# Optimization experiments

Hardware: AMD Instinct MI355X
Metric: run time of the kernel (lower is better)

Reference implementation:

```python
import jax, jax.numpy as jnp
import numpy as np

D_MODEL, H, D_FF = 512, 8, 2048
DK = D_MODEL // H
EPS = 1e-5  # torch LayerNorm default


def layer_norm(x, g, b):
    m = jnp.mean(x, axis=-1, keepdims=True)
    v = jnp.mean((x - m) ** 2, axis=-1, keepdims=True)
    return (x - m) * jax.lax.rsqrt(v + EPS) * g + b


def setup_inputs() -> dict:
    key = jax.random.key(0)
    ks = jax.random.split(key, 10)
    B, S = 8, 2048
    s = lambda fan_in: 1.0 / np.sqrt(fan_in)
    return {
        "x": jax.random.normal(ks[0], (B, S, D_MODEL), jnp.float32),
        # per-head projections stacked: [h, d_model, dk] (bias-free Project)
        "wq": jax.random.uniform(ks[1], (H, D_MODEL, DK), jnp.float32, -s(D_MODEL), s(D_MODEL)),
        "wk": jax.random.uniform(ks[2], (H, D_MODEL, DK), jnp.float32, -s(D_MODEL), s(D_MODEL)),
        "wv": jax.random.uniform(ks[3], (H, D_MODEL, DK), jnp.float32, -s(D_MODEL), s(D_MODEL)),
        "wo": jax.random.uniform(ks[4], (D_MODEL, D_MODEL), jnp.float32, -s(D_MODEL), s(D_MODEL)),
        "w1": jax.random.uniform(ks[5], (D_MODEL, D_FF), jnp.float32, -s(D_MODEL), s(D_MODEL)),
        "b1": jax.random.uniform(ks[6], (D_FF,), jnp.float32, -s(D_MODEL), s(D_MODEL)),
        "w2": jax.random.uniform(ks[7], (D_FF, D_MODEL), jnp.float32, -s(D_FF), s(D_FF)),
        "b2": jax.random.uniform(ks[8], (D_MODEL,), jnp.float32, -s(D_FF), s(D_FF)),
        "ln1_g": jnp.ones((D_MODEL,), jnp.float32),
        "ln1_b": jnp.zeros((D_MODEL,), jnp.float32),
        "ln2_g": jnp.ones((D_MODEL,), jnp.float32),
        "ln2_b": jnp.zeros((D_MODEL,), jnp.float32),
    }


def reference(x, wq, wk, wv, wo, w1, b1, w2, b2, ln1_g, ln1_b, ln2_g, ln2_b):
    B, S, D = x.shape
    # --- multi-head self-attention (8 per-head Linears fused into one einsum) ---
    q = jnp.einsum("bsd,hdk->bhsk", x, wq)
    k = jnp.einsum("bsd,hdk->bhsk", x, wk)
    v = jnp.einsum("bsd,hdk->bhsk", x, wv)
    score = jnp.einsum("bhsk,bhtk->bhst", q, k) * (1.0 / np.sqrt(DK))
    attn = jax.nn.softmax(score, axis=-1)
    heads = jnp.einsum("bhst,bhtk->bhsk", attn, v)
    concat = heads.transpose(0, 2, 1, 3).reshape(B, S, D)  # cat over heads
    mha = concat @ wo
    # dropout in eval mode -> identity
    x = layer_norm(mha + x, ln1_g, ln1_b)
    # --- feed-forward ---
    ffn = jax.nn.relu(x @ w1 + b1) @ w2 + b2
    return layer_norm(ffn + x, ln2_g, ln2_b)
```

## Files before the change

### kernel.cpp

```cpp
#include <hip/hip_runtime.h>
#include <hip/hip_bf16.h>
#include <math.h>


#define D_MODEL 512
#define NHEAD   8
#define DKH     64
#define SEQ     2048
#define BATCH   8
#define DFF     2048
#define MROWS   (BATCH * SEQ)
#define QKVLD   1536

typedef __bf16 bf16x8 __attribute__((ext_vector_type(8)));
typedef float  f32x4  __attribute__((ext_vector_type(4)));

__device__ __forceinline__ unsigned short f2bf(float f) {
    union { float f; unsigned u; } v; v.f = f;
    return (unsigned short)((v.u + 0x7FFFu + ((v.u >> 16) & 1u)) >> 16);
}

__device__ __forceinline__ unsigned cvtpk(float a, float b) {
    unsigned r;
    asm("v_cvt_pk_bf16_f32 %0, %1, %2" : "=v"(r) : "v"(a), "v"(b));
    return r;
}

__device__ __forceinline__ float fexp2(float x) {
    float r; asm("v_exp_f32 %0, %1" : "=v"(r) : "v"(x)); return r;
}

__device__ __forceinline__ f32x4 mfma16(bf16x8 a, bf16x8 b, f32x4 c) {
    return __builtin_amdgcn_mfma_f32_16x16x32_bf16(a, b, c, 0, 0, 0);
}

__device__ __forceinline__ void gld_lds16(const unsigned short* g, unsigned short* l) {
    __builtin_amdgcn_global_load_lds(
        (const __attribute__((address_space(1))) unsigned int*)g,
        (__attribute__((address_space(3))) unsigned int*)l, 16, 0, 0);
}

template<bool BIAS, bool RELU, bool RES, bool OUTF32>
__global__ __launch_bounds__(256)
void mfma_gemm(const unsigned short* __restrict__ Av,
               const unsigned short* __restrict__ Bt,
               const float* __restrict__ bias, const float* __restrict__ res,
               void* __restrict__ Cv, int Kdim, int lda, int ldc)
{
    __shared__ unsigned short As[2][128][32];
    __shared__ unsigned short Bs[2][128][32];

    const int tid  = threadIdx.x;
    const int lane = tid & 63;
    const int w    = tid >> 6;
    const int mq   = (w >> 1) << 6;
    const int nq   = (w & 1) << 6;
    const int lrow = lane & 15;
    const int g    = lane >> 4;
    const int lk   = g << 3;

    const int row0 = blockIdx.y << 7;
    const int col0 = blockIdx.x << 7;

    const int c0   = w << 5;
    const int srow = lane >> 2;
    const int scol = (lane & 3) << 3;
    const size_t aoff = (size_t)(row0 + c0 + srow) * lda  + scol;
    const size_t boff = (size_t)(col0 + c0 + srow) * Kdim + scol;

    auto stage = [&](int buf, int kt) {
        gld_lds16(Av + aoff + kt,                        &As[buf][c0     ][0]);
        gld_lds16(Av + aoff + (size_t)16 * lda  + kt,    &As[buf][c0 + 16][0]);
        gld_lds16(Bt + boff + kt,                        &Bs[buf][c0     ][0]);
        gld_lds16(Bt + boff + (size_t)16 * Kdim + kt,    &Bs[buf][c0 + 16][0]);
    };

    const f32x4 zero = {0.f, 0.f, 0.f, 0.f};
    f32x4 acc[4][4];
    #pragma unroll
    for (int i = 0; i < 4; ++i)
        #pragma unroll
        for (int j = 0; j < 4; ++j) acc[i][j] = zero;

    stage(0, 0);
    __syncthreads();

    int cur = 0;
    for (int kt = 0; kt < Kdim; kt += 32) {
        if (kt + 32 < Kdim) stage(cur ^ 1, kt + 32);

        bf16x8 af[4], bfv[4];
        #pragma unroll
        for (int mf = 0; mf < 4; ++mf)
            af[mf] = *(const bf16x8*)&As[cur][mq + mf * 16 + lrow][lk];
        #pragma unroll
        for (int nf = 0; nf < 4; ++nf)
            bfv[nf] = *(const bf16x8*)&Bs[cur][nq + nf * 16 + lrow][lk];
        #pragma unroll
        for (int mf = 0; mf < 4; ++mf)
            #pragma unroll
            for (int nf = 0; nf < 4; ++nf)
                acc[mf][nf] = mfma16(af[mf], bfv[nf], acc[mf][nf]);

        __syncthreads();
        cur ^= 1;
    }

    const int orow = row0 + mq + g * 4;
    const int ocol = col0 + nq + lrow;
    #pragma unroll
    for (int mf = 0; mf < 4; ++mf) {
        #pragma unroll
        for (int nf = 0; nf < 4; ++nf) {
            const int cc = ocol + nf * 16;
            float bv = 0.f;
            if constexpr (BIAS) bv = bias[cc];
            float v[4];
            #pragma unroll
            for (int r = 0; r < 4; ++r) {
                const int rr = orow + mf * 16 + r;
                v[r] = acc[mf][nf][r];
                if constexpr (BIAS) v[r] += bv;
                if constexpr (RELU) v[r] = fmaxf(v[r], 0.f);
                if constexpr (RES)  v[r] += res[(size_t)rr * ldc + cc];
                if constexpr (OUTF32) ((float*)Cv)[(size_t)rr * ldc + cc] = v[r];
            }
            if constexpr (!OUTF32) {
                const unsigned u01 = cvtpk(v[0], v[1]);
                const unsigned u23 = cvtpk(v[2], v[3]);
                unsigned short* cp = (unsigned short*)Cv + (size_t)(orow + mf * 16) * ldc + cc;
                cp[0]                 = (unsigned short)u01;
                cp[(size_t)ldc]       = (unsigned short)(u01 >> 16);
                cp[(size_t)ldc * 2]   = (unsigned short)u23;
                cp[(size_t)ldc * 3]   = (unsigned short)(u23 >> 16);
            }
        }
    }
}

__device__ __forceinline__ void softmax_store(
    f32x4* sacc, float* mrun, float* lpart, f32x4* oacc,
    unsigned short (*Ps)[76], int rowbase, int g, int lrow)
{
    float pmax[4];
    bool need = false;
    #pragma unroll
    for (int r = 0; r < 4; ++r) {
        pmax[r] = fmaxf(fmaxf(sacc[0][r], sacc[1][r]),
                        fmaxf(sacc[2][r], sacc[3][r]));
        need |= (pmax[r] > mrun[r] + 8.f);
    }
    if (__any(need)) {
        #pragma unroll
        for (int r = 0; r < 4; ++r) {
            float mt = pmax[r];
            mt = fmaxf(mt, __shfl_xor(mt, 1, 16));
            mt = fmaxf(mt, __shfl_xor(mt, 2, 16));
            mt = fmaxf(mt, __shfl_xor(mt, 4, 16));
            mt = fmaxf(mt, __shfl_xor(mt, 8, 16));
            const float mnew = fmaxf(mrun[r], mt);
            const float alpha = fexp2(mrun[r] - mnew);
            mrun[r] = mnew;
            lpart[r] *= alpha;
            #pragma unroll
            for (int nf = 0; nf < 4; ++nf) oacc[nf][r] *= alpha;
        }
    }
    #pragma unroll
    for (int r = 0; r < 4; ++r) {
        const float p0 = fexp2(sacc[0][r] - mrun[r]);
        const float p1 = fexp2(sacc[1][r] - mrun[r]);
        const float p2 = fexp2(sacc[2][r] - mrun[r]);
        const float p3 = fexp2(sacc[3][r] - mrun[r]);
        lpart[r] += (p0 + p1) + (p2 + p3);
        uint2 u;
        u.x = cvtpk(p0, p1);
        u.y = cvtpk(p2, p3);
        *(uint2*)&Ps[rowbase + g * 4 + r][4 * lrow] = u;
    }
}

__global__ __launch_bounds__(512, 4)
void mfma_attn(unsigned short* __restrict__ qkv)
{
    __shared__ unsigned short Ks[64][72];
    __shared__ unsigned short Vt[64][72];
    __shared__ unsigned short Ps[256][76];

    const int tid  = threadIdx.x;
    const int lane = tid & 63;
    const int w    = tid >> 6;
    const int lrow = lane & 15;
    const int g    = lane >> 4;
    const int lk   = g << 3;

    const int bid  = blockIdx.x;
    const int idx  = bid >> 3;
    const int bh   = (bid & 7) * 8 + (idx & 7);
    const int b  = bh >> 3, h = bh & 7;
    const int s0 = (idx >> 3) << 8;

    unsigned short* qptr = qkv + ((size_t)(b * SEQ + s0)) * QKVLD + h * DKH;
    const unsigned short* kbase = qkv + ((size_t)(b * SEQ)) * QKVLD + 512 + h * DKH;
    const unsigned short* vbase = qkv + ((size_t)(b * SEQ)) * QKVLD + 1024 + h * DKH;

    bf16x8 qf[2][2];
    #pragma unroll
    for (int sub = 0; sub < 2; ++sub) {
        const unsigned short* qp = qptr + (size_t)(w * 32 + sub * 16 + lrow) * QKVLD;
        qf[sub][0] = *(const bf16x8*)(qp + lk);
        qf[sub][1] = *(const bf16x8*)(qp + 32 + lk);
    }

    const int kr = tid >> 3, kc = (tid & 7) << 3;
    const int vr = tid & 63, vc = (tid >> 6) << 3;
    const int cvr = ((vr & 15) << 2) | (vr >> 4);

    uint4 kreg, vreg;
    auto loadKV = [&](int t0) {
        kreg = *(const uint4*)(kbase + (size_t)(t0 + kr) * QKVLD + kc);
        vreg = *(const uint4*)(vbase + (size_t)(t0 + vr) * QKVLD + vc);
    };
    loadKV(0);

    const f32x4 zero = {0.f, 0.f, 0.f, 0.f};
    f32x4 oacc0[4], oacc1[4];
    float m0[4], l0[4], m1[4], l1[4];
    #pragma unroll
    for (int i = 0; i < 4; ++i) {
        oacc0[i] = zero; oacc1[i] = zero;
        m0[i] = -INFINITY; m1[i] = -INFINITY; l0[i] = 0.f; l1[i] = 0.f;
    }

    for (int t0 = 0; t0 < SEQ; t0 += 64) {
        __syncthreads();
        *(uint4*)&Ks[kr][kc] = kreg;
        {
            const unsigned short* vu = (const unsigned short*)&vreg;
            #pragma unroll
            for (int j = 0; j < 8; ++j) Vt[vc + j][cvr] = vu[j];
        }
        __syncthreads();

        if (t0 + 64 < SEQ) loadKV(t0 + 64);

        f32x4 s0a[4], s1a[4];
        #pragma unroll
        for (int nf = 0; nf < 4; ++nf) { s0a[nf] = zero; s1a[nf] = zero; }
        __builtin_amdgcn_s_setprio(1);
        #pragma unroll
        for (int kk = 0; kk < 2; ++kk) {
            #pragma unroll
            for (int nf = 0; nf < 4; ++nf) {
                const bf16x8 kf = *(const bf16x8*)&Ks[nf * 16 + lrow][kk * 32 + lk];
                s0a[nf] = mfma16(qf[0][kk], kf, s0a[nf]);
                s1a[nf] = mfma16(qf[1][kk], kf, s1a[nf]);
            }
        }
        __builtin_amdgcn_s_setprio(0);

        softmax_store(s0a, m0, l0, oacc0, Ps, w * 32,      g, lrow);
        softmax_store(s1a, m1, l1, oacc1, Ps, w * 32 + 16, g, lrow);

        __builtin_amdgcn_s_setprio(1);
        #pragma unroll
        for (int kk = 0; kk < 2; ++kk) {
            const bf16x8 pf0 = *(const bf16x8*)&Ps[w * 32 + lrow][kk * 32 + lk];
            const bf16x8 pf1 = *(const bf16x8*)&Ps[w * 32 + 16 + lrow][kk * 32 + lk];
            #pragma unroll
            for (int nf = 0; nf < 4; ++nf) {
                const bf16x8 vf = *(const bf16x8*)&Vt[nf * 16 + lrow][kk * 32 + lk];
                oacc0[nf] = mfma16(pf0, vf, oacc0[nf]);
                oacc1[nf] = mfma16(pf1, vf, oacc1[nf]);
            }
        }
        __builtin_amdgcn_s_setprio(0);
    }

    #pragma unroll
    for (int r = 0; r < 4; ++r) {
        float l = l0[r];
        l += __shfl_xor(l, 1, 16);
        l += __shfl_xor(l, 2, 16);
        l += __shfl_xor(l, 4, 16);
        l += __shfl_xor(l, 8, 16);
        const float inv = 1.f / l;
        #pragma unroll
        for (int nf = 0; nf < 4; ++nf)
            qptr[(size_t)(w * 32 + g * 4 + r) * QKVLD + nf * 16 + lrow] =
                f2bf(oacc0[nf][r] * inv);
    }
    #pragma unroll
    for (int r = 0; r < 4; ++r) {
        float l = l1[r];
        l += __shfl_xor(l, 1, 16);
        l += __shfl_xor(l, 2, 16);
        l += __shfl_xor(l, 4, 16);
        l += __shfl_xor(l, 8, 16);
        const float inv = 1.f / l;
        #pragma unroll
        for (int nf = 0; nf < 4; ++nf)
            qptr[(size_t)(w * 32 + 16 + g * 4 + r) * QKVLD + nf * 16 + lrow] =
                f2bf(oacc1[nf][r] * inv);
    }
}

template<bool WB>
__global__ __launch_bounds__(256)
void ln_kernel(const float* __restrict__ in, const float* __restrict__ gg,
               const float* __restrict__ bb, float* __restrict__ outf,
               unsigned short* __restrict__ outb)
{
    const int row = blockIdx.x * 4 + (threadIdx.x >> 6);
    const int lane = threadIdx.x & 63;
    const float* p = in + (size_t)row * D_MODEL;

    const float4 a = *(const float4*)(p + lane * 4);
    const float4 c = *(const float4*)(p + 256 + lane * 4);
    float sum = a.x + a.y + a.z + a.w + c.x + c.y + c.z + c.w;
    float sq  = a.x*a.x + a.y*a.y + a.z*a.z + a.w*a.w
              + c.x*c.x + c.y*c.y + c.z*c.z + c.w*c.w;
    #pragma unroll
    for (int msk = 1; msk < 64; msk <<= 1) {
        sum += __shfl_xor(sum, msk, 64);
        sq  += __shfl_xor(sq,  msk, 64);
    }
    const float mean = sum * (1.f / 512.f);
    const float var  = sq * (1.f / 512.f) - mean * mean;
    const float rs   = rsqrtf(var + 1e-5f);

    const float4 g0 = *(const float4*)(gg + lane * 4);
    const float4 g1 = *(const float4*)(gg + 256 + lane * 4);
    const float4 b0 = *(const float4*)(bb + lane * 4);
    const float4 b1 = *(const float4*)(bb + 256 + lane * 4);

    float4 o0, o1;
    o0.x = (a.x - mean) * rs * g0.x + b0.x;
    o0.y = (a.y - mean) * rs * g0.y + b0.y;
    o0.z = (a.z - mean) * rs * g0.z + b0.z;
    o0.w = (a.w - mean) * rs * g0.w + b0.w;
    o1.x = (c.x - mean) * rs * g1.x + b1.x;
    o1.y = (c.y - mean) * rs * g1.y + b1.y;
    o1.z = (c.z - mean) * rs * g1.z + b1.z;
    o1.w = (c.w - mean) * rs * g1.w + b1.w;
    *(float4*)(outf + (size_t)row * D_MODEL + lane * 4) = o0;
    *(float4*)(outf + (size_t)row * D_MODEL + 256 + lane * 4) = o1;
    if constexpr (WB) {
        uint2 pa, pb;
        pa.x = cvtpk(o0.x, o0.y);
        pa.y = cvtpk(o0.z, o0.w);
        pb.x = cvtpk(o1.x, o1.y);
        pb.y = cvtpk(o1.z, o1.w);
        *(uint2*)(outb + (size_t)row * D_MODEL + lane * 4) = pa;
        *(uint2*)(outb + (size_t)row * D_MODEL + 256 + lane * 4) = pb;
    }
}

__global__ __launch_bounds__(256)
void cast_bf16(const float* __restrict__ in, unsigned short* __restrict__ out)
{
    const size_t i = ((size_t)blockIdx.x * 256 + threadIdx.x) * 8;
    const float4 a = *(const float4*)(in + i);
    const float4 b = *(const float4*)(in + i + 4);
    uint4 o;
    o.x = cvtpk(a.x, a.y);
    o.y = cvtpk(a.z, a.w);
    o.z = cvtpk(b.x, b.y);
    o.w = cvtpk(b.z, b.w);
    *(uint4*)(out + i) = o;
}

__global__ __launch_bounds__(256)
void pack_qkv(const float* __restrict__ wq, const float* __restrict__ wk,
              const float* __restrict__ wv, unsigned short* __restrict__ Wqkv)
{
    const int idx = blockIdx.x * 256 + threadIdx.x;
    const int n = idx >> 9, d = idx & 511;
    const int h = n >> 6, c = n & 63;
    const size_t src = ((size_t)h * 512 + d) * 64 + c;
    Wqkv[idx]                 = f2bf(wq[src] * 0.18033688f);
    Wqkv[idx + 512 * 512]     = f2bf(wk[src]);
    Wqkv[idx + 2 * 512 * 512] = f2bf(wv[src]);
}

__global__ __launch_bounds__(256)
void pack_t(const float* __restrict__ in, unsigned short* __restrict__ out,
            int K, int N)
{
    const int idx = blockIdx.x * 256 + threadIdx.x;
    const int n = idx / K, k = idx % K;
    out[idx] = f2bf(in[(size_t)k * N + n]);
}

extern "C" void kernel_launch(void* const* d_in, const int* in_sizes, int n_in,
                              void* d_out, int out_size, void* d_ws, size_t ws_size,
                              hipStream_t stream)
{
    (void)in_sizes; (void)n_in; (void)out_size;

    const float* x    = (const float*)d_in[0];
    const float* wq   = (const float*)d_in[1];
    const float* wk   = (const float*)d_in[2];
    const float* wv   = (const float*)d_in[3];
    const float* wo   = (const float*)d_in[4];
    const float* w1   = (const float*)d_in[5];
    const float* b1   = (const float*)d_in[6];
    const float* w2   = (const float*)d_in[7];
    const float* b2   = (const float*)d_in[8];
    const float* ln1g = (const float*)d_in[9];
    const float* ln1b = (const float*)d_in[10];
    const float* ln2g = (const float*)d_in[11];
    const float* ln2b = (const float*)d_in[12];
    float* out = (float*)d_out;

    const size_t QKV_BYTES = (size_t)MROWS * QKVLD * 2;
    const size_t Y_BYTES   = (size_t)MROWS * D_MODEL * 4;
    unsigned char* base = (unsigned char*)d_ws;
    unsigned short* qkv  = (unsigned short*)(base);
    float*          y    = (float*)(base + QKV_BYTES);
    unsigned short* Wqkv = (unsigned short*)(base + QKV_BYTES + Y_BYTES);
    unsigned short* wo_t = Wqkv + 3 * 512 * 512;
    unsigned short* w1_t = wo_t + 512 * 512;
    unsigned short* w2_t = w1_t + 2048 * 512;
    unsigned short* hid  = w2_t + 2048 * 512;

    const size_t hid_off = (size_t)((unsigned char*)hid - base);
    const size_t avail = (ws_size > hid_off) ? (ws_size - hid_off) : 0;
    int chunk = (int)(avail / ((size_t)DFF * 2));
    chunk &= ~127;
    if (chunk > MROWS) chunk = MROWS;
    if (chunk < 128)   chunk = 128;

    float* y2 = (float*)qkv;
    unsigned short* xb  = (unsigned short*)d_out;
    unsigned short* x1b = (unsigned short*)d_out;

    pack_qkv<<<1024, 256, 0, stream>>>(wq, wk, wv, Wqkv);
    pack_t<<<(512 * 512) / 256, 256, 0, stream>>>(wo, wo_t, 512, 512);
    pack_t<<<(2048 * 512) / 256, 256, 0, stream>>>(w1, w1_t, 512, 2048);
    pack_t<<<(2048 * 512) / 256, 256, 0, stream>>>(w2, w2_t, 2048, 512);
    cast_bf16<<<(MROWS * D_MODEL) / (256 * 8), 256, 0, stream>>>(x, xb);

    const dim3 blk(256);

    mfma_gemm<false, false, false, false>
        <<<dim3(12, MROWS / 128), blk, 0, stream>>>(xb, Wqkv, nullptr, nullptr,
                                                    qkv, 512, 512, QKVLD);

    mfma_attn<<<dim3(512), dim3(512), 0, stream>>>(qkv);

    mfma_gemm<false, false, true, true>
        <<<dim3(4, MROWS / 128), blk, 0, stream>>>(qkv, wo_t, nullptr, x, y,
                                                   512, QKVLD, 512);

    ln_kernel<true><<<MROWS / 4, blk, 0, stream>>>(y, ln1g, ln1b, y, x1b);

    for (int r0 = 0; r0 < MROWS; r0 += chunk) {
        const int rows = (r0 + chunk <= MROWS) ? chunk : (MROWS - r0);
        mfma_gemm<true, true, false, false>
            <<<dim3(DFF / 128, rows / 128), blk, 0, stream>>>(
                x1b + (size_t)r0 * D_MODEL, w1_t, b1, nullptr, hid,
                512, 512, DFF);
        mfma_gemm<true, false, true, true>
            <<<dim3(4, rows / 128), blk, 0, stream>>>(
                hid, w2_t, b2, y + (size_t)r0 * D_MODEL,
                y2 + (size_t)r0 * D_MODEL, DFF, DFF, 512);
    }

    ln_kernel<false><<<MROWS / 4, blk, 0, stream>>>(y2, ln2g, ln2b, out, nullptr);
}
```

Baseline: 311.7 us.

## Widen GEMM tiles, load attention K directly, use bf16 residual, tiled weight transpose

Adds a templated N-tile width so the QKV and FFN1 GEMMs use 128x256 tiles, raising data reuse per block. The attention kernel reads K fragments directly from global memory into registers, dropping the K shared-memory staging and its barrier traffic. LN1 stops writing its fp32 output and the FFN2 epilogue adds the residual from the bf16 copy, cutting memory traffic at some precision cost. The weight transpose kernels now use a shared-memory tile so both reads and writes are coalesced.

```diff
diff --git a/kernel.cpp b/kernel.cpp
--- a/kernel.cpp
+++ b/kernel.cpp
@@ -20,6 +20,11 @@
     return (unsigned short)((v.u + 0x7FFFu + ((v.u >> 16) & 1u)) >> 16);
 }
 
+__device__ __forceinline__ float bf2f(unsigned short u) {
+    union { unsigned u; float f; } v; v.u = (unsigned)u << 16;
+    return v.f;
+}
+
 __device__ __forceinline__ unsigned cvtpk(float a, float b) {
     unsigned r;
     asm("v_cvt_pk_bf16_f32 %0, %1, %2" : "=v"(r) : "v"(a), "v"(b));
@@ -40,47 +45,51 @@
         (__attribute__((address_space(3))) unsigned int*)l, 16, 0, 0);
 }
 
-template<bool BIAS, bool RELU, bool RES, bool OUTF32>
+template<int NF, bool BIAS, bool RELU, int RESMODE, bool OUTF32>
 __global__ __launch_bounds__(256)
 void mfma_gemm(const unsigned short* __restrict__ Av,
                const unsigned short* __restrict__ Bt,
-               const float* __restrict__ bias, const float* __restrict__ res,
+               const float* __restrict__ bias, const void* __restrict__ resv,
                void* __restrict__ Cv, int Kdim, int lda, int ldc)
 {
+    constexpr int BN = NF * 32;
     __shared__ unsigned short As[2][128][32];
-    __shared__ unsigned short Bs[2][128][32];
+    __shared__ unsigned short Bs[2][BN][32];
 
     const int tid  = threadIdx.x;
     const int lane = tid & 63;
     const int w    = tid >> 6;
     const int mq   = (w >> 1) << 6;
-    const int nq   = (w & 1) << 6;
+    const int nq   = (w & 1) * (NF * 16);
     const int lrow = lane & 15;
     const int g    = lane >> 4;
     const int lk   = g << 3;
 
     const int row0 = blockIdx.y << 7;
-    const int col0 = blockIdx.x << 7;
-
-    const int c0   = w << 5;
+    const int col0 = blockIdx.x * BN;
+
+    const int c0a  = w << 5;
+    const int c0b  = w * (BN / 4);
     const int srow = lane >> 2;
     const int scol = (lane & 3) << 3;
-    const size_t aoff = (size_t)(row0 + c0 + srow) * lda  + scol;
-    const size_t boff = (size_t)(col0 + c0 + srow) * Kdim + scol;
+    const size_t aoff = (size_t)(row0 + c0a + srow) * lda  + scol;
+    const size_t boff = (size_t)(col0 + c0b + srow) * Kdim + scol;
 
     auto stage = [&](int buf, int kt) {
-        gld_lds16(Av + aoff + kt,                        &As[buf][c0     ][0]);
-        gld_lds16(Av + aoff + (size_t)16 * lda  + kt,    &As[buf][c0 + 16][0]);
-        gld_lds16(Bt + boff + kt,                        &Bs[buf][c0     ][0]);
-        gld_lds16(Bt + boff + (size_t)16 * Kdim + kt,    &Bs[buf][c0 + 16][0]);
+        gld_lds16(Av + aoff + kt,                     &As[buf][c0a     ][0]);
+        gld_lds16(Av + aoff + (size_t)16 * lda + kt,  &As[buf][c0a + 16][0]);
+        #pragma unroll
+        for (int j = 0; j < BN / 64; ++j)
+            gld_lds16(Bt + boff + (size_t)(16 * j) * Kdim + kt,
+                      &Bs[buf][c0b + 16 * j][0]);
     };
 
     const f32x4 zero = {0.f, 0.f, 0.f, 0.f};
-    f32x4 acc[4][4];
+    f32x4 acc[4][NF];
     #pragma unroll
     for (int i = 0; i < 4; ++i)
         #pragma unroll
-        for (int j = 0; j < 4; ++j) acc[i][j] = zero;
+        for (int j = 0; j < NF; ++j) acc[i][j] = zero;
 
     stage(0, 0);
     __syncthreads();
@@ -89,18 +98,17 @@
     for (int kt = 0; kt < Kdim; kt += 32) {
         if (kt + 32 < Kdim) stage(cur ^ 1, kt + 32);
 
-        bf16x8 af[4], bfv[4];
+        bf16x8 af[4];
         #pragma unroll
         for (int mf = 0; mf < 4; ++mf)
             af[mf] = *(const bf16x8*)&As[cur][mq + mf * 16 + lrow][lk];
         #pragma unroll
-        for (int nf = 0; nf < 4; ++nf)
-            bfv[nf] = *(const bf16x8*)&Bs[cur][nq + nf * 16 + lrow][lk];
-        #pragma unroll
-        for (int mf = 0; mf < 4; ++mf)
-            #pragma unroll
-            for (int nf = 0; nf < 4; ++nf)
-                acc[mf][nf] = mfma16(af[mf], bfv[nf], acc[mf][nf]);
+        for (int nf = 0; nf < NF; ++nf) {
+            const bf16x8 bf = *(const bf16x8*)&Bs[cur][nq + nf * 16 + lrow][lk];
+            #pragma unroll
+            for (int mf = 0; mf < 4; ++mf)
+                acc[mf][nf] = mfma16(af[mf], bf, acc[mf][nf]);
+        }
 
         __syncthreads();
         cur ^= 1;
@@ -111,7 +119,7 @@
     #pragma unroll
     for (int mf = 0; mf < 4; ++mf) {
         #pragma unroll
-        for (int nf = 0; nf < 4; ++nf) {
+        for (int nf = 0; nf < NF; ++nf) {
             const int cc = ocol + nf * 16;
             float bv = 0.f;
             if constexpr (BIAS) bv = bias[cc];
@@ -122,7 +130,10 @@
                 v[r] = acc[mf][nf][r];
                 if constexpr (BIAS) v[r] += bv;
                 if constexpr (RELU) v[r] = fmaxf(v[r], 0.f);
-                if constexpr (RES)  v[r] += res[(size_t)rr * ldc + cc];
+                if constexpr (RESMODE == 1)
+                    v[r] += ((const float*)resv)[(size_t)rr * ldc + cc];
+                if constexpr (RESMODE == 2)
+                    v[r] += bf2f(((const unsigned short*)resv)[(size_t)rr * ldc + cc]);
                 if constexpr (OUTF32) ((float*)Cv)[(size_t)rr * ldc + cc] = v[r];
             }
             if constexpr (!OUTF32) {
@@ -183,7 +194,6 @@
 __global__ __launch_bounds__(512, 4)
 void mfma_attn(unsigned short* __restrict__ qkv)
 {
-    __shared__ unsigned short Ks[64][72];
     __shared__ unsigned short Vt[64][72];
     __shared__ unsigned short Ps[256][76];
 
@@ -212,16 +222,14 @@
         qf[sub][1] = *(const bf16x8*)(qp + 32 + lk);
     }
 
-    const int kr = tid >> 3, kc = (tid & 7) << 3;
     const int vr = tid & 63, vc = (tid >> 6) << 3;
     const int cvr = ((vr & 15) << 2) | (vr >> 4);
 
-    uint4 kreg, vreg;
-    auto loadKV = [&](int t0) {
-        kreg = *(const uint4*)(kbase + (size_t)(t0 + kr) * QKVLD + kc);
+    uint4 vreg;
+    auto loadV = [&](int t0) {
         vreg = *(const uint4*)(vbase + (size_t)(t0 + vr) * QKVLD + vc);
     };
-    loadKV(0);
+    loadV(0);
 
     const f32x4 zero = {0.f, 0.f, 0.f, 0.f};
     f32x4 oacc0[4], oacc1[4];
@@ -233,8 +241,15 @@
     }
 
     for (int t0 = 0; t0 < SEQ; t0 += 64) {
+        bf16x8 kf[2][4];
+        #pragma unroll
+        for (int kk = 0; kk < 2; ++kk)
+            #pragma unroll
+            for (int nf = 0; nf < 4; ++nf)
+                kf[kk][nf] = *(const bf16x8*)(
+                    kbase + (size_t)(t0 + nf * 16 + lrow) * QKVLD + kk * 32 + lk);
+
         __syncthreads();
-        *(uint4*)&Ks[kr][kc] = kreg;
         {
             const unsigned short* vu = (const unsigned short*)&vreg;
             #pragma unroll
@@ -242,7 +257,7 @@
         }
         __syncthreads();
 
-        if (t0 + 64 < SEQ) loadKV(t0 + 64);
+        if (t0 + 64 < SEQ) loadV(t0 + 64);
 
         f32x4 s0a[4], s1a[4];
         #pragma unroll
@@ -252,9 +267,8 @@
         for (int kk = 0; kk < 2; ++kk) {
             #pragma unroll
             for (int nf = 0; nf < 4; ++nf) {
-                const bf16x8 kf = *(const bf16x8*)&Ks[nf * 16 + lrow][kk * 32 + lk];
-                s0a[nf] = mfma16(qf[0][kk], kf, s0a[nf]);
-                s1a[nf] = mfma16(qf[1][kk], kf, s1a[nf]);
+                s0a[nf] = mfma16(qf[0][kk], kf[kk][nf], s0a[nf]);
+                s1a[nf] = mfma16(qf[1][kk], kf[kk][nf], s1a[nf]);
             }
         }
         __builtin_amdgcn_s_setprio(0);
@@ -305,7 +319,7 @@
     }
 }
 
-template<bool WB>
+template<bool WF32, bool WB16>
 __global__ __launch_bounds__(256)
 void ln_kernel(const float* __restrict__ in, const float* __restrict__ gg,
                const float* __restrict__ bb, float* __restrict__ outf,
@@ -343,9 +357,11 @@
     o1.y = (c.y - mean) * rs * g1.y + b1.y;
     o1.z = (c.z - mean) * rs * g1.z + b1.z;
     o1.w = (c.w - mean) * rs * g1.w + b1.w;
-    *(float4*)(outf + (size_t)row * D_MODEL + lane * 4) = o0;
-    *(float4*)(outf + (size_t)row * D_MODEL + 256 + lane * 4) = o1;
-    if constexpr (WB) {
+    if constexpr (WF32) {
+        *(float4*)(outf + (size_t)row * D_MODEL + lane * 4) = o0;
+        *(float4*)(outf + (size_t)row * D_MODEL + 256 + lane * 4) = o1;
+    }
+    if constexpr (WB16) {
         uint2 pa, pb;
         pa.x = cvtpk(o0.x, o0.y);
         pa.y = cvtpk(o0.z, o0.w);
@@ -387,9 +403,16 @@
 void pack_t(const float* __restrict__ in, unsigned short* __restrict__ out,
             int K, int N)
 {
-    const int idx = blockIdx.x * 256 + threadIdx.x;
-    const int n = idx / K, k = idx % K;
-    out[idx] = f2bf(in[(size_t)k * N + n]);
+    __shared__ float t[32][33];
+    const int kb = blockIdx.x << 5, nb = blockIdx.y << 5;
+    const int c = threadIdx.x & 31, r0 = threadIdx.x >> 5;
+    #pragma unroll
+    for (int j = 0; j < 32; j += 8)
+        t[r0 + j][c] = in[(size_t)(kb + r0 + j) * N + nb + c];
+    __syncthreads();
+    #pragma unroll
+    for (int j = 0; j < 32; j += 8)
+        out[(size_t)(nb + r0 + j) * K + kb + c] = f2bf(t[c][r0 + j]);
 }
 
 extern "C" void kernel_launch(void* const* d_in, const int* in_sizes, int n_in,
@@ -436,36 +459,38 @@
     unsigned short* x1b = (unsigned short*)d_out;
 
     pack_qkv<<<1024, 256, 0, stream>>>(wq, wk, wv, Wqkv);
-    pack_t<<<(512 * 512) / 256, 256, 0, stream>>>(wo, wo_t, 512, 512);
-    pack_t<<<(2048 * 512) / 256, 256, 0, stream>>>(w1, w1_t, 512, 2048);
-    pack_t<<<(2048 * 512) / 256, 256, 0, stream>>>(w2, w2_t, 2048, 512);
+    pack_t<<<dim3(16, 16), 256, 0, stream>>>(wo, wo_t, 512, 512);
+    pack_t<<<dim3(16, 64), 256, 0, stream>>>(w1, w1_t, 512, 2048);
+    pack_t<<<dim3(64, 16), 256, 0, stream>>>(w2, w2_t, 2048, 512);
     cast_bf16<<<(MROWS * D_MODEL) / (256 * 8), 256, 0, stream>>>(x, xb);
 
     const dim3 blk(256);
 
-    mfma_gemm<false, false, false, false>
-        <<<dim3(12, MROWS / 128), blk, 0, stream>>>(xb, Wqkv, nullptr, nullptr,
-                                                    qkv, 512, 512, QKVLD);
+    mfma_gemm<8, false, false, 0, false>
+        <<<dim3(6, MROWS / 128), blk, 0, stream>>>(xb, Wqkv, nullptr, nullptr,
+                                                   qkv, 512, 512, QKVLD);
 
     mfma_attn<<<dim3(512), dim3(512), 0, stream>>>(qkv);
 
-    mfma_gemm<false, false, true, true>
+    mfma_gemm<4, false, false, 1, true>
         <<<dim3(4, MROWS / 128), blk, 0, stream>>>(qkv, wo_t, nullptr, x, y,
                                                    512, QKVLD, 512);
 
-    ln_kernel<true><<<MROWS / 4, blk, 0, stream>>>(y, ln1g, ln1b, y, x1b);
+    ln_kernel<false, true><<<MROWS / 4, blk, 0, stream>>>(y, ln1g, ln1b,
+                                                          nullptr, x1b);
 
     for (int r0 = 0; r0 < MROWS; r0 += chunk) {
         const int rows = (r0 + chunk <= MROWS) ? chunk : (MROWS - r0);
-        mfma_gemm<true, true, false, false>
-            <<<dim3(DFF / 128, rows / 128), blk, 0, stream>>>(
+        mfma_gemm<8, true, true, 0, false>
+            <<<dim3(8, rows / 128), blk, 0, stream>>>(
                 x1b + (size_t)r0 * D_MODEL, w1_t, b1, nullptr, hid,
                 512, 512, DFF);
-        mfma_gemm<true, false, true, true>
+        mfma_gemm<4, true, false, 2, true>
             <<<dim3(4, rows / 128), blk, 0, stream>>>(
-                hid, w2_t, b2, y + (size_t)r0 * D_MODEL,
+                hid, w2_t, b2, x1b + (size_t)r0 * D_MODEL,
                 y2 + (size_t)r0 * D_MODEL, DFF, DFF, 512);
     }
 
-    ln_kernel<false><<<MROWS / 4, blk, 0, stream>>>(y2, ln2g, ln2b, out, nullptr);
-}
+    ln_kernel<true, false><<<MROWS / 4, blk, 0, stream>>>(y2, ln2g, ln2b,
+                                                          out, nullptr);
+}
```

Result: slower. 444.2 us (+42.5%).
